# Kernel optimization log

Hardware: AMD Instinct MI355X
Metric: run time of the kernel (lower is better)

The kernel has to match this reference:

```python
import jax, jax.numpy as jnp
import numpy as np
from jax import lax

GROUPS = 32  # in_channels // reduction_ratio


def setup_inputs() -> dict:
    key = jax.random.key(0)
    ks = jax.random.split(key, 12)
    B, C, H, W = 4, 256, 64, 64
    Cr = C // 8  # 32
    s = lambda k, shape, sc: jax.random.normal(k, shape, dtype=jnp.float32) * sc
    return {
        "x": s(ks[0], (B, C, H, W), 1.0),
        "wq": s(ks[1], (C, C), 0.05),          # 1x1 query conv + folded BN
        "bq": s(ks[2], (C,), 0.05),
        "wv": s(ks[3], (C, C), 0.05),          # 1x1 value conv + folded BN
        "bv": s(ks[4], (C,), 0.05),
        "w_adj1": s(ks[5], (Cr, C // GROUPS, 3), 0.1),   # grouped Conv1d OIH
        "b_adj1": s(ks[6], (Cr,), 0.05),
        "w_adj2": s(ks[7], (2 * Cr, Cr, 3), 0.1),        # Conv1d + folded BN1d
        "b_adj2": s(ks[8], (2 * Cr,), 0.05),
        "gamma": s(ks[9], (1,), 1.0),
        "w_co": s(ks[10], (C, C // 2, 4, 4), 0.05),      # ConvTranspose2d IOHW
        "b_co": s(ks[11], (C // 2,), 0.05),
    }


def reference(x, wq, bq, wv, bv, w_adj1, b_adj1, w_adj2, b_adj2, gamma, w_co, b_co):
    B, C, H, W = x.shape
    HW = H * W
    dn1 = ("NCH", "OIH", "NCH")

    # query path: 1x1 conv (+BN folded) -> [B, C, HW]
    q = jnp.einsum("oc,bchw->bohw", wq, x).reshape(B, C, HW) + bq[None, :, None]
    # conv_adj: grouped Conv1d k=3 p=1, then Conv1d k=3 p=1 (+BN1d folded)
    q = lax.conv_general_dilated(q, w_adj1, (1,), ((1, 1),),
                                 dimension_numbers=dn1,
                                 feature_group_count=GROUPS) + b_adj1[None, :, None]
    q = lax.conv_general_dilated(q, w_adj2, (1,), ((1, 1),),
                                 dimension_numbers=dn1) + b_adj2[None, :, None]
    q = q.reshape(B, C // 8, 2, HW)  # [B, Cr, 2, HW]
    query_y = q[:, :, 0, :]          # [B, Cr, HW]
    key_y = q[:, :, 1, :]            # [B, Cr, HW]

    # attention: [B, HW, HW]
    attn = jnp.einsum("bcn,bcm->bnm", query_y, key_y)
    attn_f = jax.nn.softmax(attn, axis=0)  # softmax over BATCH (faithful to source)
    attn_b = jax.nn.softmax(attn, axis=1)  # softmax over first HW axis

    # value path
    value = jnp.einsum("oc,bchw->bohw", wv, x).reshape(B, C, HW) + bv[None, :, None]

    # fusion[b,c,n] = sum_m value[b,c,m] * attn[b,n,m]
    fusion = jnp.einsum("bcm,bnm->bcn", value, attn_f + attn_b)
    fusion = gamma * fusion

    # AdaptiveAvgPool2d(1) on the 3D [B,C,HW] tensor == global mean per batch sample
    spatial = jnp.mean(x, axis=(1, 2, 3))  # [B]
    fusion = fusion * spatial[:, None, None]

    fusion = fusion.reshape(B, C, H, W) + x

    # ConvTranspose2d(C, C//2, k=4, s=2, p=1): flip kernel, swap I/O, input-dilated conv
    wt = jnp.flip(w_co, (2, 3)).transpose(1, 0, 2, 3)  # [out, in, 4, 4]
    out = lax.conv_general_dilated(fusion, wt, (1, 1), ((2, 2), (2, 2)),
                                   lhs_dilation=(2, 2),
                                   dimension_numbers=("NCHW", "OIHW", "NCHW"))
    out = out + b_co[None, :, None, None]  # [B, C//2, 2H, 2W]
    return out
```

## Files before the change

### kernel.cpp

```cpp
#include <hip/hip_runtime.h>

#define BN 4
#define CC 256
#define NN 4096
#define CR 32
#define OCH 128
#define SEGS 8

typedef float f32x4 __attribute__((ext_vector_type(4)));
typedef short short8 __attribute__((ext_vector_type(8)));
typedef unsigned short u16x8 __attribute__((ext_vector_type(8)));
typedef unsigned short u16x4 __attribute__((ext_vector_type(4)));

__device__ __forceinline__ unsigned short f2b(float f) {
  unsigned u = __builtin_bit_cast(unsigned, f);
  u += 0x7fff + ((u >> 16) & 1);
  return (unsigned short)(u >> 16);
}
__device__ __forceinline__ float b2f(unsigned short h) {
  unsigned u = ((unsigned)h) << 16;
  return __builtin_bit_cast(float, u);
}

__global__ __launch_bounds__(256) void k_wcast(const float* __restrict__ wq,
    const float* __restrict__ wv, unsigned short* __restrict__ wqb,
    unsigned short* __restrict__ wvb) {
  const int gid = (blockIdx.x * 256 + threadIdx.x) * 4;
  const float* src = blockIdx.y ? wv : wq;
  unsigned short* dst = blockIdx.y ? wvb : wqb;
  const float4 v = *(const float4*)(src + gid);
  u16x4 o; o[0] = f2b(v.x); o[1] = f2b(v.y); o[2] = f2b(v.z); o[3] = f2b(v.w);
  *(u16x4*)(dst + gid) = o;
}

__global__ __launch_bounds__(256) void k_xt(const float* __restrict__ x,
    unsigned short* __restrict__ xt, float* __restrict__ part2) {
  __shared__ unsigned short T[64][65];
  __shared__ float red[256];
  const int b = blockIdx.z, c0 = blockIdx.y * 64, n0 = blockIdx.x * 64;
  const int t = threadIdx.x;
  float s = 0.f;
  for (int idx = t; idx < 4096; idx += 256) {
    int i = idx >> 6, j = idx & 63;
    const float v = x[((size_t)(b * CC + c0 + i)) * NN + n0 + j];
    s += v;
    T[i][j] = f2b(v);
  }
  __syncthreads();
  for (int idx = t; idx < 4096; idx += 256) {
    int j = idx >> 6, i = idx & 63;
    xt[((size_t)(b * NN + n0 + j)) * CC + c0 + i] = T[i][j];
  }
  red[t] = s;
  __syncthreads();
  for (int d = 128; d > 0; d >>= 1) {
    if (t < d) red[t] += red[t + d];
    __syncthreads();
  }
  if (t == 0) part2[b * 256 + blockIdx.y * 64 + blockIdx.x] = red[0];
}

__global__ void k_spatial2(const float* __restrict__ part2, float* __restrict__ spatial) {
  const int b = blockIdx.x;
  const int t = threadIdx.x;
  __shared__ float red[256];
  red[t] = part2[b * 256 + t];
  __syncthreads();
  for (int d = 128; d > 0; d >>= 1) {
    if (t < d) red[t] += red[t + d];
    __syncthreads();
  }
  if (t == 0) spatial[b] = red[0] * (1.0f / ((float)CC * NN));
}

__global__ __launch_bounds__(256) void k_projm(const unsigned short* __restrict__ xt,
    const unsigned short* __restrict__ wqb, const float* __restrict__ bq,
    const unsigned short* __restrict__ wvb, const float* __restrict__ bv,
    unsigned short* __restrict__ q1b, unsigned short* __restrict__ Vb) {
  const int b = blockIdx.y, n0 = blockIdx.x * 32, which = blockIdx.z;
  const unsigned short* W = which ? wvb : wqb;
  const float* bias = which ? bv : bq;
  unsigned short* out = which ? Vb : q1b;
  const int t = threadIdx.x;
  const int w = t >> 6, l = t & 63;
  const int lo = l & 15, hi = l >> 4;
  const int oc0 = w * 64;
  f32x4 acc[4][2];
#pragma unroll
  for (int ct = 0; ct < 4; ++ct)
#pragma unroll
    for (int nt = 0; nt < 2; ++nt) acc[ct][nt] = (f32x4){0.f, 0.f, 0.f, 0.f};
  const unsigned short* wb = W + (size_t)(oc0 + lo) * CC + hi * 8;
  const unsigned short* xb = xt + ((size_t)(b * NN + n0 + lo)) * CC + hi * 8;
#pragma unroll
  for (int k0 = 0; k0 < CC; k0 += 32) {
    short8 aw[4], bx[2];
#pragma unroll
    for (int ct = 0; ct < 4; ++ct) aw[ct] = *(const short8*)(wb + ct * 16 * CC + k0);
#pragma unroll
    for (int nt = 0; nt < 2; ++nt) bx[nt] = *(const short8*)(xb + nt * 16 * CC + k0);
#pragma unroll
    for (int ct = 0; ct < 4; ++ct)
#pragma unroll
      for (int nt = 0; nt < 2; ++nt)
        acc[ct][nt] = __builtin_amdgcn_mfma_f32_16x16x32_bf16(aw[ct], bx[nt], acc[ct][nt], 0, 0, 0);
  }
#pragma unroll
  for (int ct = 0; ct < 4; ++ct) {
#pragma unroll
    for (int r = 0; r < 4; ++r) {
      const int c = oc0 + ct * 16 + hi * 4 + r;
      const float bvv = bias[c];
#pragma unroll
      for (int nt = 0; nt < 2; ++nt)
        out[((size_t)(b * CC + c)) * NN + n0 + nt * 16 + lo] = f2b(acc[ct][nt][r] + bvv);
    }
  }
}

__global__ __launch_bounds__(256) void k_adj1(const unsigned short* __restrict__ q1,
    const float* __restrict__ w1, const float* __restrict__ b1,
    float* __restrict__ q2) {
  const int gid = blockIdx.x * 256 + threadIdx.x;
  const int n8 = gid & 511;
  const int o = (gid >> 9) & 31;
  const int b = gid >> 14;
  const int n0 = n8 * 8;
  const unsigned short* base = q1 + ((size_t)b * CC + o * 8) * NN;
  float accv[8];
  const float bias = b1[o];
#pragma unroll
  for (int j = 0; j < 8; ++j) accv[j] = bias;
#pragma unroll
  for (int i = 0; i < 8; ++i) {
    const unsigned short* r = base + (size_t)i * NN;
    const u16x8 v = *(const u16x8*)(r + n0);
    float f[10];
    f[0] = (n0 > 0) ? b2f(r[n0 - 1]) : 0.f;
#pragma unroll
    for (int j = 0; j < 8; ++j) f[j + 1] = b2f(v[j]);
    f[9] = (n0 + 8 < NN) ? b2f(r[n0 + 8]) : 0.f;
    const float wa = w1[o * 24 + i * 3 + 0];
    const float wb = w1[o * 24 + i * 3 + 1];
    const float wc = w1[o * 24 + i * 3 + 2];
#pragma unroll
    for (int j = 0; j < 8; ++j) accv[j] += wa * f[j] + wb * f[j + 1] + wc * f[j + 2];
  }
  float4* dst = (float4*)&q2[((size_t)b * CR + o) * NN + n0];
  dst[0] = make_float4(accv[0], accv[1], accv[2], accv[3]);
  dst[1] = make_float4(accv[4], accv[5], accv[6], accv[7]);
}

__global__ __launch_bounds__(256) void k_adj2(const float* __restrict__ q2,
    const float* __restrict__ w2, const float* __restrict__ b2,
    unsigned short* __restrict__ Qt, unsigned short* __restrict__ Kt) {
  __shared__ float q2s[32][66];
  __shared__ float w2t[96][64];
  __shared__ float b2s[64];
  const int b = blockIdx.y, n0 = blockIdx.x * 64;
  const int t = threadIdx.x;
  for (int idx = t; idx < 32 * 66; idx += 256) {
    int c = idx / 66, nn = idx % 66;
    int n = n0 + nn - 1;
    q2s[c][nn] = (n >= 0 && n < NN) ? q2[((size_t)b * CR + c) * NN + n] : 0.f;
  }
  for (int idx = t; idx < 96 * 64; idx += 256) {
    int k = idx & 63, ct = idx >> 6;
    w2t[ct][k] = w2[k * 96 + ct];
  }
  if (t < 64) b2s[t] = b2[t];
  __syncthreads();
  const int nn = t & 63, kh = t >> 6;
  float acc[16];
#pragma unroll
  for (int i = 0; i < 16; ++i) acc[i] = b2s[kh * 16 + i];
  for (int c = 0; c < 32; ++c) {
    const float x0 = q2s[c][nn], x1 = q2s[c][nn + 1], x2 = q2s[c][nn + 2];
    const float* wa = &w2t[c * 3 + 0][kh * 16];
    const float* wb = &w2t[c * 3 + 1][kh * 16];
    const float* wc = &w2t[c * 3 + 2][kh * 16];
#pragma unroll
    for (int i = 0; i < 16; ++i)
      acc[i] += wa[i] * x0 + wb[i] * x1 + wc[i] * x2;
  }
  const size_t row = ((size_t)b * NN + n0 + nn) * 32;
  u16x8 qo, ko;
#pragma unroll
  for (int i = 0; i < 8; ++i) {
    qo[i] = f2b(acc[2 * i] * 1.44269504f);
    ko[i] = f2b(acc[2 * i + 1]);
  }
  *(u16x8*)(Qt + row + kh * 8) = qo;
  *(u16x8*)(Kt + row + kh * 8) = ko;
}

__global__ __launch_bounds__(512) void k_colstatm(const unsigned short* __restrict__ Qt,
    const unsigned short* __restrict__ Kt, float* __restrict__ psum) {
  __shared__ float CS[2][4][64];
  const int m0 = blockIdx.x * 64, seg = blockIdx.y;
  const int t = threadIdx.x;
  const int w = t >> 6, l = t & 63;
  const int lo = l & 15, hi = l >> 4;
  const int mt = w & 3, nt2 = w >> 2;
  const f32x4 zero4 = (f32x4){0.f, 0.f, 0.f, 0.f};
  short8 kf[4];
#pragma unroll
  for (int bb = 0; bb < 4; ++bb)
    kf[bb] = *(const short8*)(Kt + ((size_t)(bb * NN + m0 + mt * 16 + lo)) * 32 + hi * 8);
  float colacc[4] = {0.f, 0.f, 0.f, 0.f};
  for (int ch = 0; ch < 8; ++ch) {
    const int nb = seg * 512 + ch * 64;
    short8 qf[2][4];
#pragma unroll
    for (int pos = 0; pos < 2; ++pos)
#pragma unroll
      for (int bb = 0; bb < 4; ++bb)
        qf[pos][bb] = *(const short8*)(Qt + ((size_t)(bb * NN + nb + (nt2 * 2 + pos) * 16 + lo)) * 32 + hi * 8);
#pragma unroll
    for (int pos = 0; pos < 2; ++pos) {
#pragma unroll
      for (int bb = 0; bb < 4; ++bb) {
        const f32x4 s = __builtin_amdgcn_mfma_f32_16x16x32_bf16(qf[pos][bb], kf[bb], zero4, 0, 0, 0);
#pragma unroll
        for (int r = 0; r < 4; ++r) colacc[bb] += __builtin_amdgcn_exp2f(fminf(s[r], 86.f));
      }
    }
  }
#pragma unroll
  for (int bb = 0; bb < 4; ++bb) {
    colacc[bb] += __shfl_xor(colacc[bb], 16, 64);
    colacc[bb] += __shfl_xor(colacc[bb], 32, 64);
  }
  if (hi == 0) {
#pragma unroll
    for (int bb = 0; bb < 4; ++bb) CS[nt2][bb][mt * 16 + lo] = colacc[bb];
  }
  __syncthreads();
  if (t < 256) {
    const int bb = t >> 6, mm = t & 63;
    psum[((size_t)(bb * SEGS + seg)) * NN + m0 + mm] = CS[0][bb][mm] + CS[1][bb][mm];
  }
}

__global__ void k_rsum(const float* __restrict__ psum, float* __restrict__ rcs) {
  const int gid = blockIdx.x * 256 + threadIdx.x;
  const int b = gid >> 12, m = gid & (NN - 1);
  float S = 0.f;
#pragma unroll
  for (int s = 0; s < SEGS; ++s) S += psum[((size_t)(b * SEGS + s)) * NN + m];
  rcs[gid] = 1.0f / S;
}

__global__ __launch_bounds__(512, 4) void k_fused6(const unsigned short* __restrict__ Qt,
    const unsigned short* __restrict__ Kt, const unsigned short* __restrict__ Vb,
    const float* __restrict__ x, const float* __restrict__ rcs,
    const float* __restrict__ gamma, const float* __restrict__ spatial,
    unsigned short* __restrict__ fusb) {
  __shared__ unsigned short Pool[256 * 64 + 2 * 2304];
  unsigned short* VsB = Pool;
  unsigned short* AsB = Pool + 256 * 64;
  const int id = blockIdx.x;
  const int b = (id & 7) >> 1;
  const int ntile = ((id >> 3) << 1) | (id & 1);
  const int n0 = ntile * 32;
  const int t = threadIdx.x;
  const int w = t >> 6, l = t & 63;
  const int lo = l & 15, hi = l >> 4;
  const int mt = w & 3, ns = w >> 2;
  const f32x4 zero4 = (f32x4){0.f, 0.f, 0.f, 0.f};
  unsigned short* Vsw = VsB + w * 2048;

  short8 qf[4];
#pragma unroll
  for (int bb = 0; bb < 4; ++bb)
    qf[bb] = *(const short8*)(Qt + ((size_t)(bb * NN + n0 + ns * 16 + lo)) * 32 + hi * 8);

  f32x4 acc[2][2];
#pragma unroll
  for (int ct = 0; ct < 2; ++ct)
#pragma unroll
    for (int nt = 0; nt < 2; ++nt) acc[ct][nt] = zero4;

  const int cl_base = l >> 3, jj = l & 7;
  const unsigned short* vwave = Vb + ((size_t)(b * CC + w * 32)) * NN;
  const unsigned short* kbase = Kt + (size_t)(mt * 16 + lo) * 32 + hi * 8;
  const float* rcs_b = rcs + b * NN;
  const int as_off = (ns * 16 + lo) * 72 + mt * 16 + hi * 4;

  short8 kf[4];
#pragma unroll
  for (int bb = 0; bb < 4; ++bb)
    kf[bb] = *(const short8*)(kbase + (size_t)bb * NN * 32);
  {
    u16x8 vst[4];
#pragma unroll
    for (int q = 0; q < 4; ++q) {
      const int cl = q * 8 + cl_base;
      vst[q] = *(const u16x8*)(vwave + (size_t)cl * NN + jj * 8);
    }
    f32x4 s[4];
#pragma unroll
    for (int bb = 0; bb < 4; ++bb)
      s[bb] = __builtin_amdgcn_mfma_f32_16x16x32_bf16(kf[bb], qf[bb], zero4, 0, 0, 0);
    const f32x4 rc4 = *(const f32x4*)(rcs_b + mt * 16 + hi * 4);
    u16x4 av;
#pragma unroll
    for (int r = 0; r < 4; ++r) {
      const float e0 = __builtin_amdgcn_exp2f(fminf(s[0][r], 86.f));
      const float e1 = __builtin_amdgcn_exp2f(fminf(s[1][r], 86.f));
      const float e2 = __builtin_amdgcn_exp2f(fminf(s[2][r], 86.f));
      const float e3 = __builtin_amdgcn_exp2f(fminf(s[3][r], 86.f));
      const float eb = b == 0 ? e0 : (b == 1 ? e1 : (b == 2 ? e2 : e3));
      av[r] = f2b(eb * (__builtin_amdgcn_rcpf(e0 + e1 + e2 + e3) + rc4[r]));
    }
    *(u16x4*)&AsB[as_off] = av;
#pragma unroll
    for (int q = 0; q < 4; ++q) {
      const int cl = q * 8 + cl_base;
      *(u16x8*)&Vsw[cl * 64 + ((jj ^ (cl & 7)) << 3)] = vst[q];
    }
#pragma unroll
    for (int bb = 0; bb < 4; ++bb)
      kf[bb] = *(const short8*)(kbase + (size_t)bb * NN * 32 + (size_t)64 * 32);
  }
  __syncthreads();

  for (int ch = 0; ch < 64; ++ch) {
    const int cur = ch & 1;
    unsigned short* Asc = AsB + cur * 2304;
    unsigned short* Asn = AsB + (cur ^ 1) * 2304;
    u16x8 vst[4];
    u16x4 av;
    if (ch < 63) {
      const int m1 = (ch + 1) * 64;
#pragma unroll
      for (int q = 0; q < 4; ++q) {
        const int cl = q * 8 + cl_base;
        vst[q] = *(const u16x8*)(vwave + (size_t)cl * NN + m1 + jj * 8);
      }
      f32x4 s[4];
#pragma unroll
      for (int bb = 0; bb < 4; ++bb)
        s[bb] = __builtin_amdgcn_mfma_f32_16x16x32_bf16(kf[bb], qf[bb], zero4, 0, 0, 0);
      const f32x4 rc4 = *(const f32x4*)(rcs_b + m1 + mt * 16 + hi * 4);
#pragma unroll
      for (int r = 0; r < 4; ++r) {
        const float e0 = __builtin_amdgcn_exp2f(fminf(s[0][r], 86.f));
        const float e1 = __builtin_amdgcn_exp2f(fminf(s[1][r], 86.f));
        const float e2 = __builtin_amdgcn_exp2f(fminf(s[2][r], 86.f));
        const float e3 = __builtin_amdgcn_exp2f(fminf(s[3][r], 86.f));
        const float eb = b == 0 ? e0 : (b == 1 ? e1 : (b == 2 ? e2 : e3));
        av[r] = f2b(eb * (__builtin_amdgcn_rcpf(e0 + e1 + e2 + e3) + rc4[r]));
      }
      const int m2 = (ch < 62) ? (m1 + 64) : m1;
#pragma unroll
      for (int bb = 0; bb < 4; ++bb)
        kf[bb] = *(const short8*)(kbase + (size_t)bb * NN * 32 + (size_t)m2 * 32);
    }
#pragma unroll
    for (int kt = 0; kt < 2; ++kt) {
      short8 af[2];
#pragma unroll
      for (int nt = 0; nt < 2; ++nt)
        af[nt] = *(const short8*)&Asc[(nt * 16 + lo) * 72 + kt * 32 + hi * 8];
#pragma unroll
      for (int ct = 0; ct < 2; ++ct) {
        const int cl = ct * 16 + lo;
        const short8 vf = *(const short8*)&Vsw[cl * 64 + (((kt * 4 + hi) ^ (cl & 7)) << 3)];
#pragma unroll
        for (int nt = 0; nt < 2; ++nt)
          acc[ct][nt] = __builtin_amdgcn_mfma_f32_16x16x32_bf16(vf, af[nt], acc[ct][nt], 0, 0, 0);
      }
    }
    if (ch < 63) {
#pragma unroll
      for (int q = 0; q < 4; ++q) {
        const int cl = q * 8 + cl_base;
        *(u16x8*)&Vsw[cl * 64 + ((jj ^ (cl & 7)) << 3)] = vst[q];
      }
      *(u16x4*)&Asn[as_off] = av;
    }
    __syncthreads();
  }

  unsigned short* Fs = Pool;
  const float g = gamma[0] * spatial[b];
#pragma unroll
  for (int ct = 0; ct < 2; ++ct) {
#pragma unroll
    for (int nt = 0; nt < 2; ++nt) {
      u16x4 o4;
#pragma unroll
      for (int r = 0; r < 4; ++r) {
        const int c = w * 32 + ct * 16 + hi * 4 + r;
        const float xv = x[((size_t)(b * CC + c)) * NN + n0 + nt * 16 + lo];
        o4[r] = f2b(g * acc[ct][nt][r] + xv);
      }
      *(u16x4*)&Fs[(nt * 16 + lo) * 264 + w * 32 + ct * 16 + hi * 4] = o4;
    }
  }
  __syncthreads();
  const int iy = n0 >> 6, ix0 = n0 & 63;
  unsigned short* fb = fusb + (((size_t)(b * 66 + iy + 1)) * 66 + ix0 + 1) * 256;
#pragma unroll
  for (int q = 0; q < 2; ++q) {
    const int u = t + q * 512;
    const int nl = u >> 5, c0 = (u & 31) * 8;
    *(u16x8*)(fb + (size_t)nl * 256 + c0) = *(const u16x8*)&Fs[nl * 264 + c0];
  }
}

__global__ void k_wprep(const float* __restrict__ w_co, unsigned short* __restrict__ wbf) {
  const int gid = blockIdx.x * 256 + threadIdx.x;
  const int ic = gid & 255;
  const int o = (gid >> 8) & 127;
  const int tap = (gid >> 15) & 3;
  const int p = gid >> 17;
  const int py = p >> 1, px = p & 1;
  const int tyi = tap >> 1, txi = tap & 1;
  const int ky = py + 2 * tyi, kx = px + 2 * txi;
  wbf[gid] = f2b(w_co[(ic * 128 + o) * 16 + (3 - ky) * 4 + (3 - kx)]);
}

__global__ __launch_bounds__(512) void k_deconv(const unsigned short* __restrict__ fusb,
    const unsigned short* __restrict__ wbf, const float* __restrict__ b_co,
    float* __restrict__ out) {
  __shared__ unsigned short Fsh[5 * 66 * 36];
  __shared__ unsigned short Wsh[4 * 128 * 36];
  const int bp = blockIdx.y;
  const int b = bp >> 2, py = (bp >> 1) & 1, px = bp & 1;
  const int t = threadIdx.x;
  const int w = t >> 6, l = t & 63;
  const int lo = l & 15, hi = l >> 4;
  const int wm = w & 1, wrow = w >> 1;
  const int iy0 = blockIdx.x * 4;
  const int iy = iy0 + wrow;
  f32x4 acc[4][4];
#pragma unroll
  for (int mt = 0; mt < 4; ++mt)
#pragma unroll
    for (int nt = 0; nt < 4; ++nt) acc[mt][nt] = (f32x4){0.f, 0.f, 0.f, 0.f};
  const unsigned short* wp_base = wbf + (size_t)(bp & 3) * 4 * 128 * 256;
  const size_t frow0 = (size_t)(b * 66 + iy0 + py) * 66;

  for (int ic0 = 0; ic0 < 256; ic0 += 32) {
    __syncthreads();
#pragma unroll
    for (int pass = 0; pass < 3; ++pass) {
      const int idx = t + pass * 512;
      if (idx < 1320) {
        const int rr = idx / 264, rem = idx % 264;
        const int xxp = rem >> 2, h = rem & 3;
        const u16x8 v = *(const u16x8*)(fusb + (frow0 + (size_t)rr * 66 + xxp) * 256 + ic0 + h * 8);
        *(u16x8*)&Fsh[(rr * 66 + xxp) * 36 + h * 8] = v;
      }
    }
#pragma unroll
    for (int pass = 0; pass < 4; ++pass) {
      const int idx = t + pass * 512;
      const int tap = idx >> 9, o = (idx >> 2) & 127, h = idx & 3;
      const u16x8 v = *(const u16x8*)(wp_base + (size_t)tap * 32768 + (size_t)o * 256 + ic0 + h * 8);
      *(u16x8*)&Wsh[(tap * 128 + o) * 36 + h * 8] = v;
    }
    __syncthreads();
#pragma unroll
    for (int tap = 0; tap < 4; ++tap) {
      const int tyi = tap >> 1, txi = tap & 1;
      const int dx = px + txi - 1;
      const int rr = wrow + tyi;
      short8 a[4], bf[4];
#pragma unroll
      for (int mt = 0; mt < 4; ++mt)
        a[mt] = *(const short8*)&Wsh[(tap * 128 + wm * 64 + mt * 16 + lo) * 36 + hi * 8];
#pragma unroll
      for (int nt = 0; nt < 4; ++nt)
        bf[nt] = *(const short8*)&Fsh[(rr * 66 + nt * 16 + lo + dx + 1) * 36 + hi * 8];
#pragma unroll
      for (int mt = 0; mt < 4; ++mt)
#pragma unroll
        for (int nt = 0; nt < 4; ++nt)
          acc[mt][nt] = __builtin_amdgcn_mfma_f32_16x16x32_bf16(a[mt], bf[nt], acc[mt][nt], 0, 0, 0);
    }
  }
  const int y = 2 * iy + py;
#pragma unroll
  for (int mt = 0; mt < 4; ++mt) {
#pragma unroll
    for (int nt = 0; nt < 4; ++nt) {
#pragma unroll
      for (int r = 0; r < 4; ++r) {
        const int o = wm * 64 + mt * 16 + hi * 4 + r;
        const int xx = 2 * (nt * 16 + lo) + px;
        out[(((size_t)(b * OCH + o)) * 128 + y) * 128 + xx] = acc[mt][nt][r] + b_co[o];
      }
    }
  }
}

extern "C" void kernel_launch(void* const* d_in, const int* in_sizes, int n_in,
                              void* d_out, int out_size, void* d_ws, size_t ws_size,
                              hipStream_t stream) {
  const float* x     = (const float*)d_in[0];
  const float* wq    = (const float*)d_in[1];
  const float* bq    = (const float*)d_in[2];
  const float* wv    = (const float*)d_in[3];
  const float* bv    = (const float*)d_in[4];
  const float* w1    = (const float*)d_in[5];
  const float* b1    = (const float*)d_in[6];
  const float* w2    = (const float*)d_in[7];
  const float* b2    = (const float*)d_in[8];
  const float* gamma = (const float*)d_in[9];
  const float* w_co  = (const float*)d_in[10];
  const float* b_co  = (const float*)d_in[11];
  float* out = (float*)d_out;
  (void)in_sizes; (void)n_in; (void)out_size; (void)ws_size;

  char* p = (char*)d_ws;
  unsigned short* xt      = (unsigned short*)p; p += (size_t)BN * NN * CC * 2;
  unsigned short* q1b     = (unsigned short*)p; p += (size_t)BN * CC * NN * 2;
  float*          q2      = (float*)p;          p += (size_t)BN * CR * NN * 4;
  float*          psum    = (float*)p;          p += (size_t)BN * SEGS * NN * 4;
  float*          part2   = (float*)p;          p += (size_t)1024 * 4;
  unsigned short* Qt      = (unsigned short*)p; p += (size_t)BN * NN * 32 * 2;
  unsigned short* Kt      = (unsigned short*)p; p += (size_t)BN * NN * 32 * 2;
  unsigned short* Vb      = (unsigned short*)p; p += (size_t)BN * CC * NN * 2;
  float*          rcs     = (float*)p;          p += (size_t)BN * NN * 4;
  float*          spatial = (float*)p;          p += 256;
  unsigned short* wqb     = (unsigned short*)p; p += (size_t)CC * CC * 2;
  unsigned short* wvb     = (unsigned short*)p; p += (size_t)CC * CC * 2;
  unsigned short* wbf     = (unsigned short*)p; p += (size_t)4 * 4 * 128 * 256 * 2;
  unsigned short* fusb    = (unsigned short*)p;

  hipMemsetAsync(fusb, 0, (size_t)BN * 66 * 66 * 256 * 2, stream);

  k_wcast<<<dim3(64, 2), 256, 0, stream>>>(wq, wv, wqb, wvb);
  k_xt<<<dim3(64, 4, 4), 256, 0, stream>>>(x, xt, part2);
  k_projm<<<dim3(128, 4, 2), 256, 0, stream>>>(xt, wqb, bq, wvb, bv, q1b, Vb);
  k_adj1<<<dim3(256), 256, 0, stream>>>(q1b, w1, b1, q2);
  k_adj2<<<dim3(64, 4), 256, 0, stream>>>(q2, w2, b2, Qt, Kt);
  k_spatial2<<<dim3(4), 256, 0, stream>>>(part2, spatial);
  k_colstatm<<<dim3(64, SEGS), 512, 0, stream>>>(Qt, Kt, psum);
  k_rsum<<<dim3(64), 256, 0, stream>>>(psum, rcs);
  k_wprep<<<dim3(2048), 256, 0, stream>>>(w_co, wbf);
  k_fused6<<<dim3(512), 512, 0, stream>>>(Qt, Kt, Vb, x, rcs, gamma, spatial, fusb);
  k_deconv<<<dim3(16, 16), 512, 0, stream>>>(fusb, wbf, b_co, out);
}
```

Before: 230.0 us.

## Precompute batch-softmax denominators in stats kernel and reuse in fused attention

The column-statistics kernel now computes, for every (n,m) pair, the reciprocal of the sum over the batch of exp scores, stores it as a bf16 matrix (32 MB), and also emits per-n-tile partial column sums. The fused attention kernel then needs only one MFMA and one exp per element for its own batch instead of four, with the other three replaced by a bf16 load of the stored denominator. Occupancy hint rises from 4 to 6. This trades fused-kernel compute for a large extra global write and read, plus a longer reduction in rsum over 128 partials, and bf16 rounding of the denominator.

```diff
diff --git a/kernel.cpp b/kernel.cpp
--- a/kernel.cpp
+++ b/kernel.cpp
@@ -5,7 +5,6 @@
 #define NN 4096
 #define CR 32
 #define OCH 128
-#define SEGS 8
 
 typedef float f32x4 __attribute__((ext_vector_type(4)));
 typedef short short8 __attribute__((ext_vector_type(8)));
@@ -194,51 +193,55 @@
   *(u16x8*)(Kt + row + kh * 8) = ko;
 }
 
-__global__ __launch_bounds__(512) void k_colstatm(const unsigned short* __restrict__ Qt,
-    const unsigned short* __restrict__ Kt, float* __restrict__ psum) {
-  __shared__ float CS[2][4][64];
-  const int m0 = blockIdx.x * 64, seg = blockIdx.y;
+__global__ __launch_bounds__(512) void k_aden(const unsigned short* __restrict__ Qt,
+    const unsigned short* __restrict__ Kt, unsigned short* __restrict__ rden,
+    float* __restrict__ psum) {
+  __shared__ float psl[2][4][512];
+  const int ntile = blockIdx.x, mseg = blockIdx.y;
   const int t = threadIdx.x;
   const int w = t >> 6, l = t & 63;
   const int lo = l & 15, hi = l >> 4;
-  const int mt = w & 3, nt2 = w >> 2;
+  const int mt = w & 3, nh = w >> 2;
   const f32x4 zero4 = (f32x4){0.f, 0.f, 0.f, 0.f};
-  short8 kf[4];
+  short8 qf[4];
 #pragma unroll
   for (int bb = 0; bb < 4; ++bb)
-    kf[bb] = *(const short8*)(Kt + ((size_t)(bb * NN + m0 + mt * 16 + lo)) * 32 + hi * 8);
-  float colacc[4] = {0.f, 0.f, 0.f, 0.f};
+    qf[bb] = *(const short8*)(Qt + ((size_t)(bb * NN + ntile * 32 + nh * 16 + lo)) * 32 + hi * 8);
+  const int slot = (mt * 2 + nh) * 64 + hi * 16 + lo;
   for (int ch = 0; ch < 8; ++ch) {
-    const int nb = seg * 512 + ch * 64;
-    short8 qf[2][4];
-#pragma unroll
-    for (int pos = 0; pos < 2; ++pos)
+    const int m0 = mseg * 512 + ch * 64;
+    short8 kf[4];
+#pragma unroll
+    for (int bb = 0; bb < 4; ++bb)
+      kf[bb] = *(const short8*)(Kt + ((size_t)(bb * NN + m0 + mt * 16 + lo)) * 32 + hi * 8);
+    f32x4 s[4];
+#pragma unroll
+    for (int bb = 0; bb < 4; ++bb)
+      s[bb] = __builtin_amdgcn_mfma_f32_16x16x32_bf16(kf[bb], qf[bb], zero4, 0, 0, 0);
+    u16x4 av;
+#pragma unroll
+    for (int r = 0; r < 4; ++r) {
+      float e[4];
 #pragma unroll
       for (int bb = 0; bb < 4; ++bb)
-        qf[pos][bb] = *(const short8*)(Qt + ((size_t)(bb * NN + nb + (nt2 * 2 + pos) * 16 + lo)) * 32 + hi * 8);
-#pragma unroll
-    for (int pos = 0; pos < 2; ++pos) {
+        e[bb] = __builtin_amdgcn_exp2f(fminf(s[bb][r], 86.f));
+      av[r] = f2b(__builtin_amdgcn_rcpf(e[0] + e[1] + e[2] + e[3]));
 #pragma unroll
       for (int bb = 0; bb < 4; ++bb) {
-        const f32x4 s = __builtin_amdgcn_mfma_f32_16x16x32_bf16(qf[pos][bb], kf[bb], zero4, 0, 0, 0);
-#pragma unroll
-        for (int r = 0; r < 4; ++r) colacc[bb] += __builtin_amdgcn_exp2f(fminf(s[r], 86.f));
-      }
-    }
-  }
-#pragma unroll
-  for (int bb = 0; bb < 4; ++bb) {
-    colacc[bb] += __shfl_xor(colacc[bb], 16, 64);
-    colacc[bb] += __shfl_xor(colacc[bb], 32, 64);
-  }
-  if (hi == 0) {
-#pragma unroll
-    for (int bb = 0; bb < 4; ++bb) CS[nt2][bb][mt * 16 + lo] = colacc[bb];
-  }
-  __syncthreads();
-  if (t < 256) {
-    const int bb = t >> 6, mm = t & 63;
-    psum[((size_t)(bb * SEGS + seg)) * NN + m0 + mm] = CS[0][bb][mm] + CS[1][bb][mm];
+        float v = e[bb];
+        v += __shfl_xor(v, 1, 64);
+        v += __shfl_xor(v, 2, 64);
+        v += __shfl_xor(v, 4, 64);
+        v += __shfl_xor(v, 8, 64);
+        if (lo == 0) psl[nh][bb][ch * 64 + mt * 16 + hi * 4 + r] = v;
+      }
+    }
+    *(u16x4*)(rden + ((size_t)(ntile * 64 + mseg * 8 + ch)) * 2048 + slot * 4) = av;
+  }
+  __syncthreads();
+  for (int idx = t; idx < 2048; idx += 512) {
+    const int bb = idx >> 9, ml = idx & 511;
+    psum[((size_t)(ntile * 4 + bb)) * NN + mseg * 512 + ml] = psl[0][bb][ml] + psl[1][bb][ml];
   }
 }
 
@@ -246,16 +249,15 @@
   const int gid = blockIdx.x * 256 + threadIdx.x;
   const int b = gid >> 12, m = gid & (NN - 1);
   float S = 0.f;
-#pragma unroll
-  for (int s = 0; s < SEGS; ++s) S += psum[((size_t)(b * SEGS + s)) * NN + m];
+  for (int nt = 0; nt < 128; ++nt) S += psum[((size_t)(nt * 4 + b)) * NN + m];
   rcs[gid] = 1.0f / S;
 }
 
-__global__ __launch_bounds__(512, 4) void k_fused6(const unsigned short* __restrict__ Qt,
+__global__ __launch_bounds__(512, 6) void k_fused7(const unsigned short* __restrict__ Qt,
     const unsigned short* __restrict__ Kt, const unsigned short* __restrict__ Vb,
-    const float* __restrict__ x, const float* __restrict__ rcs,
-    const float* __restrict__ gamma, const float* __restrict__ spatial,
-    unsigned short* __restrict__ fusb) {
+    const unsigned short* __restrict__ rden, const float* __restrict__ x,
+    const float* __restrict__ rcs, const float* __restrict__ gamma,
+    const float* __restrict__ spatial, unsigned short* __restrict__ fusb) {
   __shared__ unsigned short Pool[256 * 64 + 2 * 2304];
   unsigned short* VsB = Pool;
   unsigned short* AsB = Pool + 256 * 64;
@@ -270,10 +272,7 @@
   const f32x4 zero4 = (f32x4){0.f, 0.f, 0.f, 0.f};
   unsigned short* Vsw = VsB + w * 2048;
 
-  short8 qf[4];
-#pragma unroll
-  for (int bb = 0; bb < 4; ++bb)
-    qf[bb] = *(const short8*)(Qt + ((size_t)(bb * NN + n0 + ns * 16 + lo)) * 32 + hi * 8);
+  const short8 qf = *(const short8*)(Qt + ((size_t)(b * NN + n0 + ns * 16 + lo)) * 32 + hi * 8);
 
   f32x4 acc[2][2];
 #pragma unroll
@@ -283,14 +282,13 @@
 
   const int cl_base = l >> 3, jj = l & 7;
   const unsigned short* vwave = Vb + ((size_t)(b * CC + w * 32)) * NN;
-  const unsigned short* kbase = Kt + (size_t)(mt * 16 + lo) * 32 + hi * 8;
+  const unsigned short* kbase = Kt + ((size_t)(b * NN + mt * 16 + lo)) * 32 + hi * 8;
+  const unsigned short* rdbase = rden + ((size_t)ntile * 64) * 2048
+                               + (size_t)((mt * 2 + ns) * 64 + hi * 16 + lo) * 4;
   const float* rcs_b = rcs + b * NN;
   const int as_off = (ns * 16 + lo) * 72 + mt * 16 + hi * 4;
 
-  short8 kf[4];
-#pragma unroll
-  for (int bb = 0; bb < 4; ++bb)
-    kf[bb] = *(const short8*)(kbase + (size_t)bb * NN * 32);
+  short8 kf = *(const short8*)(kbase);
   {
     u16x8 vst[4];
 #pragma unroll
@@ -298,20 +296,14 @@
       const int cl = q * 8 + cl_base;
       vst[q] = *(const u16x8*)(vwave + (size_t)cl * NN + jj * 8);
     }
-    f32x4 s[4];
-#pragma unroll
-    for (int bb = 0; bb < 4; ++bb)
-      s[bb] = __builtin_amdgcn_mfma_f32_16x16x32_bf16(kf[bb], qf[bb], zero4, 0, 0, 0);
+    const u16x4 rd4 = *(const u16x4*)(rdbase);
+    const f32x4 s = __builtin_amdgcn_mfma_f32_16x16x32_bf16(kf, qf, zero4, 0, 0, 0);
     const f32x4 rc4 = *(const f32x4*)(rcs_b + mt * 16 + hi * 4);
     u16x4 av;
 #pragma unroll
     for (int r = 0; r < 4; ++r) {
-      const float e0 = __builtin_amdgcn_exp2f(fminf(s[0][r], 86.f));
-      const float e1 = __builtin_amdgcn_exp2f(fminf(s[1][r], 86.f));
-      const float e2 = __builtin_amdgcn_exp2f(fminf(s[2][r], 86.f));
-      const float e3 = __builtin_amdgcn_exp2f(fminf(s[3][r], 86.f));
-      const float eb = b == 0 ? e0 : (b == 1 ? e1 : (b == 2 ? e2 : e3));
-      av[r] = f2b(eb * (__builtin_amdgcn_rcpf(e0 + e1 + e2 + e3) + rc4[r]));
+      const float e = __builtin_amdgcn_exp2f(fminf(s[r], 86.f));
+      av[r] = f2b(e * (b2f(rd4[r]) + rc4[r]));
     }
     *(u16x4*)&AsB[as_off] = av;
 #pragma unroll
@@ -319,9 +311,7 @@
       const int cl = q * 8 + cl_base;
       *(u16x8*)&Vsw[cl * 64 + ((jj ^ (cl & 7)) << 3)] = vst[q];
     }
-#pragma unroll
-    for (int bb = 0; bb < 4; ++bb)
-      kf[bb] = *(const short8*)(kbase + (size_t)bb * NN * 32 + (size_t)64 * 32);
+    kf = *(const short8*)(kbase + (size_t)64 * 32);
   }
   __syncthreads();
 
@@ -338,24 +328,16 @@
         const int cl = q * 8 + cl_base;
         vst[q] = *(const u16x8*)(vwave + (size_t)cl * NN + m1 + jj * 8);
       }
-      f32x4 s[4];
-#pragma unroll
-      for (int bb = 0; bb < 4; ++bb)
-        s[bb] = __builtin_amdgcn_mfma_f32_16x16x32_bf16(kf[bb], qf[bb], zero4, 0, 0, 0);
+      const u16x4 rd4 = *(const u16x4*)(rdbase + (size_t)(ch + 1) * 2048);
+      const f32x4 s = __builtin_amdgcn_mfma_f32_16x16x32_bf16(kf, qf, zero4, 0, 0, 0);
       const f32x4 rc4 = *(const f32x4*)(rcs_b + m1 + mt * 16 + hi * 4);
 #pragma unroll
       for (int r = 0; r < 4; ++r) {
-        const float e0 = __builtin_amdgcn_exp2f(fminf(s[0][r], 86.f));
-        const float e1 = __builtin_amdgcn_exp2f(fminf(s[1][r], 86.f));
-        const float e2 = __builtin_amdgcn_exp2f(fminf(s[2][r], 86.f));
-        const float e3 = __builtin_amdgcn_exp2f(fminf(s[3][r], 86.f));
-        const float eb = b == 0 ? e0 : (b == 1 ? e1 : (b == 2 ? e2 : e3));
-        av[r] = f2b(eb * (__builtin_amdgcn_rcpf(e0 + e1 + e2 + e3) + rc4[r]));
+        const float e = __builtin_amdgcn_exp2f(fminf(s[r], 86.f));
+        av[r] = f2b(e * (b2f(rd4[r]) + rc4[r]));
       }
       const int m2 = (ch < 62) ? (m1 + 64) : m1;
-#pragma unroll
-      for (int bb = 0; bb < 4; ++bb)
-        kf[bb] = *(const short8*)(kbase + (size_t)bb * NN * 32 + (size_t)m2 * 32);
+      kf = *(const short8*)(kbase + (size_t)m2 * 32);
     }
 #pragma unroll
     for (int kt = 0; kt < 2; ++kt) {
@@ -519,7 +501,6 @@
   unsigned short* xt      = (unsigned short*)p; p += (size_t)BN * NN * CC * 2;
   unsigned short* q1b     = (unsigned short*)p; p += (size_t)BN * CC * NN * 2;
   float*          q2      = (float*)p;          p += (size_t)BN * CR * NN * 4;
-  float*          psum    = (float*)p;          p += (size_t)BN * SEGS * NN * 4;
   float*          part2   = (float*)p;          p += (size_t)1024 * 4;
   unsigned short* Qt      = (unsigned short*)p; p += (size_t)BN * NN * 32 * 2;
   unsigned short* Kt      = (unsigned short*)p; p += (size_t)BN * NN * 32 * 2;
@@ -529,7 +510,9 @@
   unsigned short* wqb     = (unsigned short*)p; p += (size_t)CC * CC * 2;
   unsigned short* wvb     = (unsigned short*)p; p += (size_t)CC * CC * 2;
   unsigned short* wbf     = (unsigned short*)p; p += (size_t)4 * 4 * 128 * 256 * 2;
-  unsigned short* fusb    = (unsigned short*)p;
+  unsigned short* fusb    = (unsigned short*)p; p += (size_t)BN * 66 * 66 * 256 * 2;
+  unsigned short* rden    = (unsigned short*)p; p += (size_t)NN * NN * 2;
+  float*          psum    = (float*)xt;
 
   hipMemsetAsync(fusb, 0, (size_t)BN * 66 * 66 * 256 * 2, stream);
 
@@ -539,9 +522,9 @@
   k_adj1<<<dim3(256), 256, 0, stream>>>(q1b, w1, b1, q2);
   k_adj2<<<dim3(64, 4), 256, 0, stream>>>(q2, w2, b2, Qt, Kt);
   k_spatial2<<<dim3(4), 256, 0, stream>>>(part2, spatial);
-  k_colstatm<<<dim3(64, SEGS), 512, 0, stream>>>(Qt, Kt, psum);
+  k_aden<<<dim3(128, 8), 512, 0, stream>>>(Qt, Kt, rden, psum);
   k_rsum<<<dim3(64), 256, 0, stream>>>(psum, rcs);
   k_wprep<<<dim3(2048), 256, 0, stream>>>(w_co, wbf);
-  k_fused6<<<dim3(512), 512, 0, stream>>>(Qt, Kt, Vb, x, rcs, gamma, spatial, fusb);
+  k_fused7<<<dim3(512), 512, 0, stream>>>(Qt, Kt, Vb, rden, x, rcs, gamma, spatial, fusb);
   k_deconv<<<dim3(16, 16), 512, 0, stream>>>(fusb, wbf, b_co, out);
 }
```

Measured after the change: 242.4 us. 5.4% more time.

## Precompute batch-softmax denominators once in a separate kernel shared across batches

Applied to the files above, without the earlier changes.

Adds a kernel that computes the reciprocal of the cross-batch softmax denominator for every (n,m) pair once and stores it as bf16 in a 32 MB buffer. The fused attention kernel previously recomputed all four batch scores and exponentials in each of the four batch blocks. It now computes only its own batch's score and reads the precomputed denominator, and its occupancy hint is raised. This removes redundant MFMA and exp work but adds a large global write and read of the denominator table, and bf16-rounds the denominator.

```diff
diff --git a/kernel.cpp b/kernel.cpp
--- a/kernel.cpp
+++ b/kernel.cpp
@@ -251,11 +251,47 @@
   rcs[gid] = 1.0f / S;
 }
 
-__global__ __launch_bounds__(512, 4) void k_fused6(const unsigned short* __restrict__ Qt,
+__global__ __launch_bounds__(512) void k_aden(const unsigned short* __restrict__ Qt,
+    const unsigned short* __restrict__ Kt, unsigned short* __restrict__ rden) {
+  const int ntile = blockIdx.x, mseg = blockIdx.y;
+  const int t = threadIdx.x;
+  const int w = t >> 6, l = t & 63;
+  const int lo = l & 15, hi = l >> 4;
+  const int mt = w & 3, nh = w >> 2;
+  const f32x4 zero4 = (f32x4){0.f, 0.f, 0.f, 0.f};
+  short8 qf[4];
+#pragma unroll
+  for (int bb = 0; bb < 4; ++bb)
+    qf[bb] = *(const short8*)(Qt + ((size_t)(bb * NN + ntile * 32 + nh * 16 + lo)) * 32 + hi * 8);
+  const int slot = (mt * 2 + nh) * 64 + hi * 16 + lo;
+  for (int ch = 0; ch < 8; ++ch) {
+    const int m0 = mseg * 512 + ch * 64;
+    short8 kf[4];
+#pragma unroll
+    for (int bb = 0; bb < 4; ++bb)
+      kf[bb] = *(const short8*)(Kt + ((size_t)(bb * NN + m0 + mt * 16 + lo)) * 32 + hi * 8);
+    f32x4 s[4];
+#pragma unroll
+    for (int bb = 0; bb < 4; ++bb)
+      s[bb] = __builtin_amdgcn_mfma_f32_16x16x32_bf16(kf[bb], qf[bb], zero4, 0, 0, 0);
+    u16x4 av;
+#pragma unroll
+    for (int r = 0; r < 4; ++r) {
+      const float e0 = __builtin_amdgcn_exp2f(fminf(s[0][r], 86.f));
+      const float e1 = __builtin_amdgcn_exp2f(fminf(s[1][r], 86.f));
+      const float e2 = __builtin_amdgcn_exp2f(fminf(s[2][r], 86.f));
+      const float e3 = __builtin_amdgcn_exp2f(fminf(s[3][r], 86.f));
+      av[r] = f2b(__builtin_amdgcn_rcpf(e0 + e1 + e2 + e3));
+    }
+    *(u16x4*)(rden + ((size_t)(ntile * 64 + mseg * 8 + ch)) * 2048 + slot * 4) = av;
+  }
+}
+
+__global__ __launch_bounds__(512, 6) void k_fused7(const unsigned short* __restrict__ Qt,
     const unsigned short* __restrict__ Kt, const unsigned short* __restrict__ Vb,
-    const float* __restrict__ x, const float* __restrict__ rcs,
-    const float* __restrict__ gamma, const float* __restrict__ spatial,
-    unsigned short* __restrict__ fusb) {
+    const unsigned short* __restrict__ rden, const float* __restrict__ x,
+    const float* __restrict__ rcs, const float* __restrict__ gamma,
+    const float* __restrict__ spatial, unsigned short* __restrict__ fusb) {
   __shared__ unsigned short Pool[256 * 64 + 2 * 2304];
   unsigned short* VsB = Pool;
   unsigned short* AsB = Pool + 256 * 64;
@@ -270,10 +306,7 @@
   const f32x4 zero4 = (f32x4){0.f, 0.f, 0.f, 0.f};
   unsigned short* Vsw = VsB + w * 2048;
 
-  short8 qf[4];
-#pragma unroll
-  for (int bb = 0; bb < 4; ++bb)
-    qf[bb] = *(const short8*)(Qt + ((size_t)(bb * NN + n0 + ns * 16 + lo)) * 32 + hi * 8);
+  const short8 qf = *(const short8*)(Qt + ((size_t)(b * NN + n0 + ns * 16 + lo)) * 32 + hi * 8);
 
   f32x4 acc[2][2];
 #pragma unroll
@@ -283,14 +316,13 @@
 
   const int cl_base = l >> 3, jj = l & 7;
   const unsigned short* vwave = Vb + ((size_t)(b * CC + w * 32)) * NN;
-  const unsigned short* kbase = Kt + (size_t)(mt * 16 + lo) * 32 + hi * 8;
+  const unsigned short* kbase = Kt + ((size_t)(b * NN + mt * 16 + lo)) * 32 + hi * 8;
+  const unsigned short* rdbase = rden + ((size_t)ntile * 64) * 2048
+                               + (size_t)((mt * 2 + ns) * 64 + hi * 16 + lo) * 4;
   const float* rcs_b = rcs + b * NN;
   const int as_off = (ns * 16 + lo) * 72 + mt * 16 + hi * 4;
 
-  short8 kf[4];
-#pragma unroll
-  for (int bb = 0; bb < 4; ++bb)
-    kf[bb] = *(const short8*)(kbase + (size_t)bb * NN * 32);
+  short8 kf = *(const short8*)(kbase);
   {
     u16x8 vst[4];
 #pragma unroll
@@ -298,20 +330,14 @@
       const int cl = q * 8 + cl_base;
       vst[q] = *(const u16x8*)(vwave + (size_t)cl * NN + jj * 8);
     }
-    f32x4 s[4];
-#pragma unroll
-    for (int bb = 0; bb < 4; ++bb)
-      s[bb] = __builtin_amdgcn_mfma_f32_16x16x32_bf16(kf[bb], qf[bb], zero4, 0, 0, 0);
+    const u16x4 rd4 = *(const u16x4*)(rdbase);
+    const f32x4 s = __builtin_amdgcn_mfma_f32_16x16x32_bf16(kf, qf, zero4, 0, 0, 0);
     const f32x4 rc4 = *(const f32x4*)(rcs_b + mt * 16 + hi * 4);
     u16x4 av;
 #pragma unroll
     for (int r = 0; r < 4; ++r) {
-      const float e0 = __builtin_amdgcn_exp2f(fminf(s[0][r], 86.f));
-      const float e1 = __builtin_amdgcn_exp2f(fminf(s[1][r], 86.f));
-      const float e2 = __builtin_amdgcn_exp2f(fminf(s[2][r], 86.f));
-      const float e3 = __builtin_amdgcn_exp2f(fminf(s[3][r], 86.f));
-      const float eb = b == 0 ? e0 : (b == 1 ? e1 : (b == 2 ? e2 : e3));
-      av[r] = f2b(eb * (__builtin_amdgcn_rcpf(e0 + e1 + e2 + e3) + rc4[r]));
+      const float e = __builtin_amdgcn_exp2f(fminf(s[r], 86.f));
+      av[r] = f2b(e * (b2f(rd4[r]) + rc4[r]));
     }
     *(u16x4*)&AsB[as_off] = av;
 #pragma unroll
@@ -319,9 +345,7 @@
       const int cl = q * 8 + cl_base;
       *(u16x8*)&Vsw[cl * 64 + ((jj ^ (cl & 7)) << 3)] = vst[q];
     }
-#pragma unroll
-    for (int bb = 0; bb < 4; ++bb)
-      kf[bb] = *(const short8*)(kbase + (size_t)bb * NN * 32 + (size_t)64 * 32);
+    kf = *(const short8*)(kbase + (size_t)64 * 32);
   }
   __syncthreads();
 
@@ -338,24 +362,16 @@
         const int cl = q * 8 + cl_base;
         vst[q] = *(const u16x8*)(vwave + (size_t)cl * NN + m1 + jj * 8);
       }
-      f32x4 s[4];
-#pragma unroll
-      for (int bb = 0; bb < 4; ++bb)
-        s[bb] = __builtin_amdgcn_mfma_f32_16x16x32_bf16(kf[bb], qf[bb], zero4, 0, 0, 0);
+      const u16x4 rd4 = *(const u16x4*)(rdbase + (size_t)(ch + 1) * 2048);
+      const f32x4 s = __builtin_amdgcn_mfma_f32_16x16x32_bf16(kf, qf, zero4, 0, 0, 0);
       const f32x4 rc4 = *(const f32x4*)(rcs_b + m1 + mt * 16 + hi * 4);
 #pragma unroll
       for (int r = 0; r < 4; ++r) {
-        const float e0 = __builtin_amdgcn_exp2f(fminf(s[0][r], 86.f));
-        const float e1 = __builtin_amdgcn_exp2f(fminf(s[1][r], 86.f));
-        const float e2 = __builtin_amdgcn_exp2f(fminf(s[2][r], 86.f));
-        const float e3 = __builtin_amdgcn_exp2f(fminf(s[3][r], 86.f));
-        const float eb = b == 0 ? e0 : (b == 1 ? e1 : (b == 2 ? e2 : e3));
-        av[r] = f2b(eb * (__builtin_amdgcn_rcpf(e0 + e1 + e2 + e3) + rc4[r]));
+        const float e = __builtin_amdgcn_exp2f(fminf(s[r], 86.f));
+        av[r] = f2b(e * (b2f(rd4[r]) + rc4[r]));
       }
       const int m2 = (ch < 62) ? (m1 + 64) : m1;
-#pragma unroll
-      for (int bb = 0; bb < 4; ++bb)
-        kf[bb] = *(const short8*)(kbase + (size_t)bb * NN * 32 + (size_t)m2 * 32);
+      kf = *(const short8*)(kbase + (size_t)m2 * 32);
     }
 #pragma unroll
     for (int kt = 0; kt < 2; ++kt) {
@@ -529,7 +545,8 @@
   unsigned short* wqb     = (unsigned short*)p; p += (size_t)CC * CC * 2;
   unsigned short* wvb     = (unsigned short*)p; p += (size_t)CC * CC * 2;
   unsigned short* wbf     = (unsigned short*)p; p += (size_t)4 * 4 * 128 * 256 * 2;
-  unsigned short* fusb    = (unsigned short*)p;
+  unsigned short* fusb    = (unsigned short*)p; p += (size_t)BN * 66 * 66 * 256 * 2;
+  unsigned short* rden    = (unsigned short*)p; p += (size_t)NN * NN * 2;
 
   hipMemsetAsync(fusb, 0, (size_t)BN * 66 * 66 * 256 * 2, stream);
 
@@ -541,7 +558,8 @@
   k_spatial2<<<dim3(4), 256, 0, stream>>>(part2, spatial);
   k_colstatm<<<dim3(64, SEGS), 512, 0, stream>>>(Qt, Kt, psum);
   k_rsum<<<dim3(64), 256, 0, stream>>>(psum, rcs);
+  k_aden<<<dim3(128, 8), 512, 0, stream>>>(Qt, Kt, rden);
   k_wprep<<<dim3(2048), 256, 0, stream>>>(w_co, wbf);
-  k_fused6<<<dim3(512), 512, 0, stream>>>(Qt, Kt, Vb, x, rcs, gamma, spatial, fusb);
+  k_fused7<<<dim3(512), 512, 0, stream>>>(Qt, Kt, Vb, rden, x, rcs, gamma, spatial, fusb);
   k_deconv<<<dim3(16, 16), 512, 0, stream>>>(fusb, wbf, b_co, out);
 }
```

Measured after the change: 219.0 us. 1.05x faster.
